# Kernel tuning notes

Hardware: AMD Instinct MI355X
Metric: run time of the kernel (lower is better)

The kernel has to match this reference:

```python
import jax, jax.numpy as jnp
import numpy as np

L = 5        # num_layer
D = 128      # emb_dim
N = 100000   # nodes
E = 500000   # edges
G = 128      # graphs in batch
NUM_TYPES = 100
NUM_ATTRS = 1000
MAX_DEPTH = 21


def _bn(x, g, b):
    # training-mode BatchNorm1d statistics (per-feature over rows)
    mu = x.mean(axis=0)
    var = x.var(axis=0)
    return (x - mu) * jax.lax.rsqrt(var + 1e-5) * g + b


def setup_inputs() -> dict:
    key = jax.random.key(0)
    ks = jax.random.split(key, 24)
    inp = {}
    x0 = jax.random.randint(ks[0], (N,), 0, NUM_TYPES)
    x1 = jax.random.randint(ks[1], (N,), 0, NUM_ATTRS)
    inp['x'] = jnp.stack([x0, x1], axis=1)
    inp['node_depth'] = jax.random.randint(ks[2], (N,), 0, MAX_DEPTH)
    inp['edge_index'] = jax.random.randint(ks[3], (2, E), 0, N)
    inp['batch'] = jnp.sort(jax.random.randint(ks[4], (N,), 0, G))
    inp['edge_attr'] = jax.random.normal(ks[5], (E, 2), dtype=jnp.float32)
    s = 0.02
    inp['type_emb'] = jax.random.normal(ks[6], (NUM_TYPES, D), dtype=jnp.float32) * s
    inp['attr_emb'] = jax.random.normal(ks[7], (NUM_ATTRS, D), dtype=jnp.float32) * s
    inp['depth_emb'] = jax.random.normal(ks[8], (MAX_DEPTH, D), dtype=jnp.float32) * s
    inp['vn_emb'] = jnp.zeros((1, D), dtype=jnp.float32)  # init constant 0
    inp['eps'] = jnp.zeros((L,), dtype=jnp.float32)       # GIN eps
    inp['edge_W'] = jax.random.normal(ks[9], (L, 2, D), dtype=jnp.float32) * s
    inp['edge_b'] = jnp.zeros((L, D), dtype=jnp.float32)
    inp['gin_W1'] = jax.random.normal(ks[10], (L, D, 2 * D), dtype=jnp.float32) * s
    inp['gin_b1'] = jnp.zeros((L, 2 * D), dtype=jnp.float32)
    inp['gin_bng'] = jnp.ones((L, 2 * D), dtype=jnp.float32)
    inp['gin_bnb'] = jnp.zeros((L, 2 * D), dtype=jnp.float32)
    inp['gin_W2'] = jax.random.normal(ks[11], (L, 2 * D, D), dtype=jnp.float32) * s
    inp['gin_b2'] = jnp.zeros((L, D), dtype=jnp.float32)
    inp['bng'] = jnp.ones((L, D), dtype=jnp.float32)
    inp['bnb'] = jnp.zeros((L, D), dtype=jnp.float32)
    inp['vn_W1'] = jax.random.normal(ks[12], (L - 1, D, 2 * D), dtype=jnp.float32) * s
    inp['vn_b1'] = jnp.zeros((L - 1, 2 * D), dtype=jnp.float32)
    inp['vn_bn1g'] = jnp.ones((L - 1, 2 * D), dtype=jnp.float32)
    inp['vn_bn1b'] = jnp.zeros((L - 1, 2 * D), dtype=jnp.float32)
    inp['vn_W2'] = jax.random.normal(ks[13], (L - 1, 2 * D, D), dtype=jnp.float32) * s
    inp['vn_b2'] = jnp.zeros((L - 1, D), dtype=jnp.float32)
    inp['vn_bn2g'] = jnp.ones((L - 1, D), dtype=jnp.float32)
    inp['vn_bn2b'] = jnp.zeros((L - 1, D), dtype=jnp.float32)
    return inp


def reference(x, node_depth, edge_index, batch, edge_attr,
              type_emb, attr_emb, depth_emb, vn_emb, eps,
              edge_W, edge_b, gin_W1, gin_b1, gin_bng, gin_bnb, gin_W2, gin_b2,
              bng, bnb, vn_W1, vn_b1, vn_bn1g, vn_bn1b, vn_W2, vn_b2, vn_bn2g, vn_bn2b):
    # node encoder: type + attribute + depth embeddings  -> [N, D]
    h = type_emb[x[:, 0]] + attr_emb[x[:, 1]] + depth_emb[node_depth]
    vn = jnp.broadcast_to(vn_emb[0], (G, D))  # virtual node per graph
    src, dst = edge_index[0], edge_index[1]
    for l in range(L):
        # broadcast virtual node to its graph's nodes
        h = h + vn[batch]
        # GIN conv: aggr_j relu(h_j + edge_emb), then (1+eps)*h + aggr -> MLP
        eemb = edge_attr @ edge_W[l] + edge_b[l]            # [E, D]
        msg = jax.nn.relu(h[src] + eemb)                    # [E, D]
        aggr = jax.ops.segment_sum(msg, dst, num_segments=N)
        z = (1.0 + eps[l]) * h + aggr
        z = jax.nn.relu(_bn(z @ gin_W1[l] + gin_b1[l], gin_bng[l], gin_bnb[l]))
        z = z @ gin_W2[l] + gin_b2[l]
        hn = _bn(z, bng[l], bnb[l])                         # outer BatchNorm
        if l < L - 1:
            hn = jax.nn.relu(hn)                            # dropout=identity (eval)
            # virtual node update: global_add_pool of pre-conv h + MLP
            vt = jax.ops.segment_sum(h, batch, num_segments=G) + vn
            vt = jax.nn.relu(_bn(vt @ vn_W1[l] + vn_b1[l], vn_bn1g[l], vn_bn1b[l]))
            vn = jax.nn.relu(_bn(vt @ vn_W2[l] + vn_b2[l], vn_bn2g[l], vn_bn2b[l]))
        h = hn
    return h  # JK == 'last'
```

## Files before the change

kernel.cpp:

```cpp
#include <hip/hip_runtime.h>

#define D 128
#define GG 128
#define SLOTS 64

typedef __attribute__((ext_vector_type(8))) short bf16x8;
typedef __attribute__((ext_vector_type(4))) float f32x4;

__device__ __forceinline__ short f2bf(float f) {
  unsigned u = __float_as_uint(f);
  unsigned r = u + 0x7fffu + ((u >> 16) & 1u);
  return (short)(r >> 16);
}
__device__ __forceinline__ float bf2f(unsigned short h) {
  return __uint_as_float(((unsigned)h) << 16);
}

__device__ __forceinline__ void bn_coef(float s, float q, float invn, float g, float b,
                                        float& sc, float& sh) {
  float mu = s * invn;
  float var = q * invn - mu * mu;
  sc = g * rsqrtf(var + 1e-5f);
  sh = b - mu * sc;
}

__global__ void k_deg(int E, const int* __restrict__ dst, int* __restrict__ deg) {
  int e = blockIdx.x * 256 + threadIdx.x;
  if (e < E) atomicAdd(&deg[dst[e]], 1);
}

__global__ void k_scan1(int N, const int* __restrict__ deg,
                        int* __restrict__ incl, int* __restrict__ blksum) {
  __shared__ int s[256];
  int t = threadIdx.x, n = blockIdx.x * 256 + t;
  int v = (n < N) ? deg[n] : 0;
  s[t] = v; __syncthreads();
  for (int off = 1; off < 256; off <<= 1) {
    int x = (t >= off) ? s[t - off] : 0;
    __syncthreads();
    s[t] += x;
    __syncthreads();
  }
  if (n < N) incl[n] = s[t];
  if (t == 255) blksum[blockIdx.x] = s[255];
}

__global__ void k_scan2(int B, int* __restrict__ blksum) {
  __shared__ int s[512];
  int t = threadIdx.x;
  s[t] = (t < B) ? blksum[t] : 0;
  __syncthreads();
  for (int off = 1; off < 512; off <<= 1) {
    int x = (t >= off) ? s[t - off] : 0;
    __syncthreads();
    s[t] += x;
    __syncthreads();
  }
  if (t < B) blksum[t] = s[t];
}

__global__ void k_scan3(int N, const int* __restrict__ incl, const int* __restrict__ blksum,
                        const int* __restrict__ deg, int* __restrict__ row_ptr) {
  int n = blockIdx.x * 256 + threadIdx.x;
  if (n >= N) return;
  int b = n >> 8;
  int off = (b > 0) ? blksum[b - 1] : 0;
  row_ptr[n] = off + incl[n] - deg[n];
  if (n == N - 1) row_ptr[N] = off + incl[n];
}

__global__ void k_fill(int E, const int* __restrict__ src, const int* __restrict__ dst,
                       const float* __restrict__ ea, const int* __restrict__ row_ptr,
                       int* __restrict__ cursor, int* __restrict__ src_sorted,
                       float2* __restrict__ ea_sorted) {
  int e = blockIdx.x * 256 + threadIdx.x;
  if (e >= E) return;
  int d = dst[e];
  int pos = row_ptr[d] + atomicAdd(&cursor[d], 1);
  src_sorted[pos] = src[e];
  ea_sorted[pos] = make_float2(ea[2 * e], ea[2 * e + 1]);
}

__global__ void k_pack(const float* __restrict__ gW1, const float* __restrict__ gW2,
                       short* __restrict__ w1t, short* __restrict__ w2t) {
  int id = blockIdx.x * 256 + threadIdx.x;
  if (id < 5 * 256 * 128) {
    int l = id / 32768, r = id % 32768, n = r / 128, k = r % 128;
    w1t[id] = f2bf(gW1[l * 32768 + k * 256 + n]);
  }
  if (id < 5 * 128 * 256) {
    int l = id / 32768, r = id % 32768, n = r / 256, k = r % 256;
    w2t[id] = f2bf(gW2[l * 32768 + k * 128 + n]);
  }
}

__global__ void k_coef(int NC, float invn,
                       const float* __restrict__ part_s, const float* __restrict__ part_q,
                       const float* __restrict__ g, const float* __restrict__ b,
                       float* __restrict__ sc, float* __restrict__ sh,
                       float* __restrict__ outs, float* __restrict__ outq) {
  int t = threadIdx.x;
  if (t >= NC) return;
  float s = 0.f, q = 0.f;
  #pragma unroll 4
  for (int i = 0; i < SLOTS; ++i) {
    s += part_s[i * NC + t];
    q += part_q[i * NC + t];
  }
  if (outs) { outs[t] = s; outq[t] = q; }
  if (g) {
    float a, c;
    bn_coef(s, q, invn, g[t], b[t], a, c);
    sc[t] = a; sh[t] = c;
  }
}

__global__ void k_nodeprep(int N, int mode,
    const int* __restrict__ x, const int* __restrict__ depth,
    const float* __restrict__ te, const float* __restrict__ ae, const float* __restrict__ de,
    const short* __restrict__ z2, const float* __restrict__ s2, const float* __restrict__ q2,
    const float* __restrict__ g2, const float* __restrict__ b2,
    int vn_mode, const float* __restrict__ vne,
    const float* __restrict__ t2v, const float* __restrict__ vs2, const float* __restrict__ vq2,
    const float* __restrict__ vg2, const float* __restrict__ vb2,
    const int* __restrict__ batch,
    short* __restrict__ h2, float* __restrict__ vt_pool, int do_pool)
{
  int t = threadIdx.x;
  int d = t & (D - 1);
  int lane = t >> 7;
  int n0 = blockIdx.x * 16;
  float invn = 1.0f / (float)N;
  float sc = 0.f, sh = 0.f, vsc = 0.f, vsh = 0.f;
  if (mode == 1)    bn_coef(s2[d], q2[d], invn, g2[d], b2[d], sc, sh);
  if (vn_mode == 1) bn_coef(vs2[d], vq2[d], 1.0f / (float)GG, vg2[d], vb2[d], vsc, vsh);
  int cur = -1; float acc = 0.f;
  for (int k = 0; k < 8; ++k) {
    int n = n0 + lane * 8 + k;
    if (n >= N) break;
    float hv;
    if (mode == 0) {
      hv = te[x[2 * n] * D + d] + ae[x[2 * n + 1] * D + d] + de[depth[n] * D + d];
    } else {
      float z = bf2f((unsigned short)z2[(size_t)n * D + d]);
      hv = fmaxf(z * sc + sh, 0.f);
    }
    int g = batch[n];
    float vnv;
    if (vn_mode == 0) vnv = vne[d];
    else { float tv = t2v[g * D + d]; vnv = fmaxf(tv * vsc + vsh, 0.f); }
    float h = hv + vnv;
    h2[(size_t)n * D + d] = f2bf(h);
    if (do_pool) {
      if (g != cur) {
        if (cur >= 0) atomicAdd(&vt_pool[cur * D + d], acc);
        cur = g; acc = 0.f;
      }
      acc += h;
    }
  }
  if (do_pool && cur >= 0) atomicAdd(&vt_pool[cur * D + d], acc);
}

__global__ void __launch_bounds__(256) k_gather(int N,
    const int* __restrict__ row_ptr, const int* __restrict__ src_sorted,
    const float2* __restrict__ ea_sorted,
    const float* __restrict__ ew, const float* __restrict__ eb,
    const float* __restrict__ epsp,
    const short* __restrict__ h2, short* __restrict__ am)
{
  int t = threadIdx.x;
  int w = t >> 6, l = t & 63;
  int n = blockIdx.x * 4 + w;
  if (n >= N) return;
  int d0 = l * 2;
  float ew00 = ew[d0], ew01 = ew[d0 + 1];
  float ew10 = ew[D + d0], ew11 = ew[D + d0 + 1];
  float eb0 = eb[d0], eb1 = eb[d0 + 1];
  float ep1 = 1.0f + epsp[0];
  unsigned hv = *(const unsigned*)(h2 + (size_t)n * D + d0);
  float acc0 = ep1 * bf2f((unsigned short)(hv & 0xffff));
  float acc1 = ep1 * bf2f((unsigned short)(hv >> 16));
  int beg = row_ptr[n], end = row_ptr[n + 1];
  for (int i = beg; i < end; ++i) {
    int s = src_sorted[i];
    float2 a = ea_sorted[i];
    unsigned sv = *(const unsigned*)(h2 + (size_t)s * D + d0);
    acc0 += fmaxf(bf2f((unsigned short)(sv & 0xffff)) + a.x * ew00 + a.y * ew10 + eb0, 0.f);
    acc1 += fmaxf(bf2f((unsigned short)(sv >> 16))    + a.x * ew01 + a.y * ew11 + eb1, 0.f);
  }
  unsigned o = ((unsigned)(unsigned short)f2bf(acc0)) |
               (((unsigned)(unsigned short)f2bf(acc1)) << 16);
  *(unsigned*)(am + (size_t)n * D + d0) = o;
}

template<int STAGES, int BN_A>
__global__ void __launch_bounds__(256) k_gemm(int N, int NC,
    const short* __restrict__ A, int strideA,
    const short* __restrict__ Bt, int strideB,
    const float* __restrict__ bias,
    const float* __restrict__ scA, const float* __restrict__ shA,
    short* __restrict__ C, int strideC,
    float* __restrict__ part_s, float* __restrict__ part_q)
{
  __shared__ __align__(16) char As[16384];
  __shared__ __align__(16) char Bs[32768];
  __shared__ float cs[128], cq[128];
  int t = threadIdx.x;
  int m0 = blockIdx.x * 64;
  int n0 = blockIdx.y * 128;
  int w = t >> 6, l = t & 63;
  int wr = w & 1, wc = w >> 1;
  int lm = l & 15, kb = l >> 4;

  if (t < 128) { cs[t] = 0.f; cq[t] = 0.f; }

  f32x4 acc[2][4];
  #pragma unroll
  for (int j = 0; j < 4; ++j) {
    float bj = bias[n0 + wc * 64 + j * 16 + lm];
    acc[0][j] = (f32x4){bj, bj, bj, bj};
    acc[1][j] = (f32x4){bj, bj, bj, bj};
  }

  #pragma unroll
  for (int s = 0; s < STAGES; ++s) {
    if (s > 0) __syncthreads();
    #pragma unroll
    for (int r = 0; r < 4; ++r) {
      int p = (r * 256 + t) * 16;
      int row = p >> 8, c = p & 255;
      int gr = m0 + row; if (gr > N - 1) gr = N - 1;
      bf16x8 v = *(const bf16x8*)((const char*)A + (size_t)gr * strideA + s * 256 + c);
      if (BN_A) {
        int kg = s * 128 + (c >> 1);
        float4 s0 = *(const float4*)(scA + kg);
        float4 s1 = *(const float4*)(scA + kg + 4);
        float4 h0 = *(const float4*)(shA + kg);
        float4 h1 = *(const float4*)(shA + kg + 4);
        v[0] = f2bf(fmaxf(bf2f((unsigned short)v[0]) * s0.x + h0.x, 0.f));
        v[1] = f2bf(fmaxf(bf2f((unsigned short)v[1]) * s0.y + h0.y, 0.f));
        v[2] = f2bf(fmaxf(bf2f((unsigned short)v[2]) * s0.z + h0.z, 0.f));
        v[3] = f2bf(fmaxf(bf2f((unsigned short)v[3]) * s0.w + h0.w, 0.f));
        v[4] = f2bf(fmaxf(bf2f((unsigned short)v[4]) * s1.x + h1.x, 0.f));
        v[5] = f2bf(fmaxf(bf2f((unsigned short)v[5]) * s1.y + h1.y, 0.f));
        v[6] = f2bf(fmaxf(bf2f((unsigned short)v[6]) * s1.z + h1.z, 0.f));
        v[7] = f2bf(fmaxf(bf2f((unsigned short)v[7]) * s1.w + h1.w, 0.f));
      }
      *(bf16x8*)(As + row * 256 + (c ^ ((row & 7) << 4))) = v;
    }
    #pragma unroll
    for (int r = 0; r < 8; ++r) {
      int p = (r * 256 + t) * 16;
      int col = p >> 8, c = p & 255;
      bf16x8 v = *(const bf16x8*)((const char*)Bt + (size_t)(n0 + col) * strideB + s * 256 + c);
      *(bf16x8*)(Bs + col * 256 + (c ^ ((col & 7) << 4))) = v;
    }
    __syncthreads();
    #pragma unroll
    for (int ks = 0; ks < 4; ++ks) {
      int kB = ks * 64 + kb * 16;
      bf16x8 fa[2], fb[4];
      #pragma unroll
      for (int i = 0; i < 2; ++i) {
        int rl = wr * 32 + i * 16 + lm;
        fa[i] = *(const bf16x8*)(As + rl * 256 + (kB ^ ((rl & 7) << 4)));
      }
      #pragma unroll
      for (int j = 0; j < 4; ++j) {
        int cl = wc * 64 + j * 16 + lm;
        fb[j] = *(const bf16x8*)(Bs + cl * 256 + (kB ^ ((cl & 7) << 4)));
      }
      #pragma unroll
      for (int i = 0; i < 2; ++i)
        #pragma unroll
        for (int j = 0; j < 4; ++j)
          acc[i][j] = __builtin_amdgcn_mfma_f32_16x16x32_bf16(fa[i], fb[j], acc[i][j], 0, 0, 0);
    }
  }

  #pragma unroll
  for (int j = 0; j < 4; ++j) {
    int col = n0 + wc * 64 + j * 16 + lm;
    float sv = 0.f, qv = 0.f;
    #pragma unroll
    for (int i = 0; i < 2; ++i) {
      #pragma unroll
      for (int r = 0; r < 4; ++r) {
        int row = m0 + wr * 32 + i * 16 + kb * 4 + r;
        float vv = acc[i][j][r];
        if (row < N) { C[(size_t)row * strideC + col] = f2bf(vv); sv += vv; qv += vv * vv; }
      }
    }
    sv += __shfl_xor(sv, 16); sv += __shfl_xor(sv, 32);
    qv += __shfl_xor(qv, 16); qv += __shfl_xor(qv, 32);
    if (l < 16) { atomicAdd(&cs[col - n0], sv); atomicAdd(&cq[col - n0], qv); }
  }
  __syncthreads();
  if (t < 128) {
    int slot = (blockIdx.x + blockIdx.y) & (SLOTS - 1);
    atomicAdd(&part_s[(size_t)slot * NC + n0 + t], cs[t]);
    atomicAdd(&part_q[(size_t)slot * NC + n0 + t], cq[t]);
  }
}

__global__ void k_vn1(const float* __restrict__ vt_pool,
    int vn_mode, const float* __restrict__ vne, const float* __restrict__ t2v,
    const float* __restrict__ vs2, const float* __restrict__ vq2,
    const float* __restrict__ vg2, const float* __restrict__ vb2,
    const float* __restrict__ W1, const float* __restrict__ b1,
    float* __restrict__ t1v, float* __restrict__ s1, float* __restrict__ q1)
{
  __shared__ float vrow[128];
  int g = blockIdx.x, t = threadIdx.x;
  if (t < 128) {
    float vnv;
    if (vn_mode == 0) vnv = vne[t];
    else {
      float sc, sh;
      bn_coef(vs2[t], vq2[t], 1.f / (float)GG, vg2[t], vb2[t], sc, sh);
      vnv = fmaxf(t2v[g * D + t] * sc + sh, 0.f);
    }
    vrow[t] = vt_pool[g * D + t] + vnv;
  }
  __syncthreads();
  float acc = b1[t];
  for (int k = 0; k < 128; ++k) acc += vrow[k] * W1[k * 256 + t];
  t1v[g * 256 + t] = acc;
  atomicAdd(&s1[t], acc);
  atomicAdd(&q1[t], acc * acc);
}

__global__ void k_vn2(const float* __restrict__ t1v,
    const float* __restrict__ s1, const float* __restrict__ q1,
    const float* __restrict__ g1, const float* __restrict__ b1bn,
    const float* __restrict__ W2, const float* __restrict__ b2,
    float* __restrict__ t2v, float* __restrict__ s2, float* __restrict__ q2)
{
  __shared__ float p[256];
  int g = blockIdx.x, t = threadIdx.x;
  for (int u = t; u < 256; u += 128) {
    float sc, sh;
    bn_coef(s1[u], q1[u], 1.f / (float)GG, g1[u], b1bn[u], sc, sh);
    p[u] = fmaxf(t1v[g * 256 + u] * sc + sh, 0.f);
  }
  __syncthreads();
  float acc = b2[t];
  for (int k = 0; k < 256; ++k) acc += p[k] * W2[k * D + t];
  t2v[g * D + t] = acc;
  atomicAdd(&s2[t], acc);
  atomicAdd(&q2[t], acc * acc);
}

__global__ void k_out(int N, const short* __restrict__ z2,
    const float* __restrict__ s2, const float* __restrict__ q2,
    const float* __restrict__ g2, const float* __restrict__ b2, float* __restrict__ out)
{
  long long idx = (long long)blockIdx.x * 256 + threadIdx.x;
  long long base = idx * 2;
  if (base >= (long long)N * D) return;
  int d = (int)(base & (D - 1));
  float invn = 1.f / (float)N;
  unsigned v = *(const unsigned*)(z2 + base);
  float sc0, sh0, sc1, sh1;
  bn_coef(s2[d], q2[d], invn, g2[d], b2[d], sc0, sh0);
  bn_coef(s2[d + 1], q2[d + 1], invn, g2[d + 1], b2[d + 1], sc1, sh1);
  out[base]     = bf2f((unsigned short)(v & 0xffff)) * sc0 + sh0;
  out[base + 1] = bf2f((unsigned short)(v >> 16))    * sc1 + sh1;
}

extern "C" void kernel_launch(void* const* d_in, const int* in_sizes, int n_in,
                              void* d_out, int out_size, void* d_ws, size_t ws_size,
                              hipStream_t stream) {
  const int*   x     = (const int*)d_in[0];
  const int*   depth = (const int*)d_in[1];
  const int*   eidx  = (const int*)d_in[2];
  const int*   batch = (const int*)d_in[3];
  const float* ea    = (const float*)d_in[4];
  const float* te    = (const float*)d_in[5];
  const float* aemb  = (const float*)d_in[6];
  const float* de    = (const float*)d_in[7];
  const float* vne   = (const float*)d_in[8];
  const float* epsp  = (const float*)d_in[9];
  const float* eW    = (const float*)d_in[10];
  const float* eb    = (const float*)d_in[11];
  const float* gW1   = (const float*)d_in[12];
  const float* gb1   = (const float*)d_in[13];
  const float* gbng  = (const float*)d_in[14];
  const float* gbnb  = (const float*)d_in[15];
  const float* gW2   = (const float*)d_in[16];
  const float* gb2   = (const float*)d_in[17];
  const float* bng   = (const float*)d_in[18];
  const float* bnb   = (const float*)d_in[19];
  const float* vW1   = (const float*)d_in[20];
  const float* vb1   = (const float*)d_in[21];
  const float* vbn1g = (const float*)d_in[22];
  const float* vbn1b = (const float*)d_in[23];
  const float* vW2   = (const float*)d_in[24];
  const float* vb2   = (const float*)d_in[25];
  const float* vbn2g = (const float*)d_in[26];
  const float* vbn2b = (const float*)d_in[27];

  int N = in_sizes[0] / 2;
  int E = in_sizes[2] / 2;
  const int* src = eidx;
  const int* dst = eidx + E;

  char* wsp = (char*)d_ws;
  auto alloc = [&](size_t bytes) -> char* {
    char* p = wsp; wsp += (bytes + 15) & ~(size_t)15; return p;
  };
  short* h2         = (short*)alloc((size_t)N * 128 * 2);
  short* am         = (short*)alloc((size_t)N * 128 * 2);
  short* t1         = (short*)alloc((size_t)N * 256 * 2);
  short* z2         = (short*)alloc((size_t)N * 128 * 2);
  short* w1t        = (short*)alloc((size_t)5 * 256 * 128 * 2);
  short* w2t        = (short*)alloc((size_t)5 * 128 * 256 * 2);
  int*   row_ptr    = (int*)alloc((size_t)(N + 1) * 4);
  int*   incl       = (int*)alloc((size_t)N * 4);
  int*   blksum     = (int*)alloc(512 * 4);
  int*   src_sorted = (int*)alloc((size_t)E * 4);
  float2* ea_sorted = (float2*)alloc((size_t)E * 8);
  float* sc1        = (float*)alloc(256 * 4);
  float* sh1        = (float*)alloc(256 * 4);
  char* zero_base = wsp;
  int*  deg    = (int*)alloc((size_t)N * 4);
  int*  cursor = (int*)alloc((size_t)N * 4);
  float* sp = (float*)wsp;
  float *p1s[5], *p1q[5], *p2s[5], *p2q[5], *s2s[5], *q2s[5];
  for (int l = 0; l < 5; ++l) {
    p1s[l]=sp; sp+=SLOTS*256; p1q[l]=sp; sp+=SLOTS*256;
    p2s[l]=sp; sp+=SLOTS*128; p2q[l]=sp; sp+=SLOTS*128;
    s2s[l]=sp; sp+=128; q2s[l]=sp; sp+=128;
  }
  float *vt[4], *t1v[4], *t2v[4], *vs1[4], *vq1[4], *vs2[4], *vq2[4];
  for (int l = 0; l < 4; ++l) {
    vt[l]=sp;  sp+=GG*D;
    t1v[l]=sp; sp+=GG*256;
    t2v[l]=sp; sp+=GG*D;
    vs1[l]=sp; sp+=256; vq1[l]=sp; sp+=256;
    vs2[l]=sp; sp+=128; vq2[l]=sp; sp+=128;
  }
  size_t zero_bytes = (size_t)((char*)sp - zero_base);
  hipMemsetAsync(zero_base, 0, zero_bytes, stream);

  int eblk = (E + 255) / 256;
  int nblk = (N + 255) / 256;
  int B = nblk;
  k_deg<<<eblk, 256, 0, stream>>>(E, dst, deg);
  k_scan1<<<nblk, 256, 0, stream>>>(N, deg, incl, blksum);
  k_scan2<<<1, 512, 0, stream>>>(B, blksum);
  k_scan3<<<nblk, 256, 0, stream>>>(N, incl, blksum, deg, row_ptr);
  k_fill<<<eblk, 256, 0, stream>>>(E, src, dst, ea, row_ptr, cursor, src_sorted, ea_sorted);

  k_pack<<<(5 * 256 * 128 + 255) / 256, 256, 0, stream>>>(gW1, gW2, w1t, w2t);

  int nblk_a = (N + 15) / 16;
  int nblk_gth = (N + 3) / 4;
  int nblk_m = (N + 63) / 64;
  float invn = 1.f / (float)N;

  for (int l = 0; l < 5; ++l) {
    int mode    = (l == 0) ? 0 : 1;
    int vn_mode = (l == 0) ? 0 : 1;
    int do_pool = (l < 4) ? 1 : 0;
    const float* ps2  = (l > 0) ? s2s[l-1] : s2s[0];
    const float* pq2  = (l > 0) ? q2s[l-1] : q2s[0];
    const float* pg2  = (l > 0) ? bng + (l-1)*D : bng;
    const float* pb2  = (l > 0) ? bnb + (l-1)*D : bnb;
    const float* pt2v = (l > 0) ? t2v[l-1] : t2v[0];
    const float* pvs2 = (l > 0) ? vs2[l-1] : vs2[0];
    const float* pvq2 = (l > 0) ? vq2[l-1] : vq2[0];
    const float* pvg2 = (l > 0) ? vbn2g + (l-1)*D : vbn2g;
    const float* pvb2 = (l > 0) ? vbn2b + (l-1)*D : vbn2b;

    k_nodeprep<<<nblk_a, 256, 0, stream>>>(N, mode, x, depth, te, aemb, de,
        z2, ps2, pq2, pg2, pb2,
        vn_mode, vne, pt2v, pvs2, pvq2, pvg2, pvb2,
        batch, h2, do_pool ? vt[l] : vt[0], do_pool);

    k_gather<<<nblk_gth, 256, 0, stream>>>(N, row_ptr, src_sorted, ea_sorted,
        eW + l*2*D, eb + l*D, epsp + l, h2, am);

    k_gemm<1, 0><<<dim3(nblk_m, 2), 256, 0, stream>>>(N, 256,
        am, 256, w1t + (size_t)l*256*128, 256,
        gb1 + l*256, nullptr, nullptr, t1, 256, p1s[l], p1q[l]);

    k_coef<<<1, 256, 0, stream>>>(256, invn, p1s[l], p1q[l],
        gbng + l*256, gbnb + l*256, sc1, sh1, nullptr, nullptr);

    k_gemm<2, 1><<<dim3(nblk_m, 1), 256, 0, stream>>>(N, 128,
        t1, 512, w2t + (size_t)l*128*256, 512,
        gb2 + l*128, sc1, sh1, z2, 128, p2s[l], p2q[l]);

    k_coef<<<1, 256, 0, stream>>>(128, invn, p2s[l], p2q[l],
        nullptr, nullptr, nullptr, nullptr, s2s[l], q2s[l]);

    if (l < 4) {
      k_vn1<<<GG, 256, 0, stream>>>(vt[l], vn_mode, vne, pt2v, pvs2, pvq2, pvg2, pvb2,
          vW1 + (size_t)l*128*256, vb1 + l*256, t1v[l], vs1[l], vq1[l]);
      k_vn2<<<GG, 128, 0, stream>>>(t1v[l], vs1[l], vq1[l],
          vbn1g + l*256, vbn1b + l*256,
          vW2 + (size_t)l*256*128, vb2 + l*128, t2v[l], vs2[l], vq2[l]);
    }
  }

  k_out<<<(int)(((long long)N * D / 2 + 255) / 256), 256, 0, stream>>>(N, z2, s2s[4], q2s[4],
      bng + 4*D, bnb + 4*D, (float*)d_out);
}
```

Measured before the change: 998.3 us.

## Pad CSR to multiples of four, pack edge records, enlarge GEMM tiles, fuse BN coef

Pads each node's in-degree to a multiple of four, using sentinel edges that point at an extra h2 row holding -1e30, so the ReLU of a padded message is zero. Source index and edge attributes are packed into one int4 record per edge, which lets the gather loop unroll by four with fewer index loads. The GEMM tile grows from 64 to 128 rows with launch bounds of 2, and the first BatchNorm coefficient reduction moves into the second GEMM's prologue, removing one k_coef launch per layer. The cost is more gathered bytes per edge (16 vs 12), extra padded iterations, and more registers and LDS per GEMM block. Every second-GEMM block also repeats the 64-slot reduction.

```diff
diff --git a/kernel.cpp b/kernel.cpp
--- a/kernel.cpp
+++ b/kernel.cpp
@@ -33,7 +33,7 @@
                         int* __restrict__ incl, int* __restrict__ blksum) {
   __shared__ int s[256];
   int t = threadIdx.x, n = blockIdx.x * 256 + t;
-  int v = (n < N) ? deg[n] : 0;
+  int v = (n < N) ? ((deg[n] + 3) & ~3) : 0;
   s[t] = v; __syncthreads();
   for (int off = 1; off < 256; off <<= 1) {
     int x = (t >= off) ? s[t - off] : 0;
@@ -65,20 +65,32 @@
   if (n >= N) return;
   int b = n >> 8;
   int off = (b > 0) ? blksum[b - 1] : 0;
-  row_ptr[n] = off + incl[n] - deg[n];
+  int pdeg = (deg[n] + 3) & ~3;
+  row_ptr[n] = off + incl[n] - pdeg;
   if (n == N - 1) row_ptr[N] = off + incl[n];
 }
 
 __global__ void k_fill(int E, const int* __restrict__ src, const int* __restrict__ dst,
                        const float* __restrict__ ea, const int* __restrict__ row_ptr,
-                       int* __restrict__ cursor, int* __restrict__ src_sorted,
-                       float2* __restrict__ ea_sorted) {
+                       int* __restrict__ cursor, int4* __restrict__ er) {
   int e = blockIdx.x * 256 + threadIdx.x;
   if (e >= E) return;
   int d = dst[e];
   int pos = row_ptr[d] + atomicAdd(&cursor[d], 1);
-  src_sorted[pos] = src[e];
-  ea_sorted[pos] = make_float2(ea[2 * e], ea[2 * e + 1]);
+  er[pos] = make_int4(src[e] << 8, __float_as_int(ea[2 * e]), __float_as_int(ea[2 * e + 1]), 0);
+}
+
+__global__ void k_padfill(int N, const int* __restrict__ deg, const int* __restrict__ row_ptr,
+                          int4* __restrict__ er) {
+  int n = blockIdx.x * 256 + threadIdx.x;
+  if (n >= N) return;
+  int s = row_ptr[n] + deg[n], e = row_ptr[n + 1];
+  int4 pad = make_int4(N << 8, 0, 0, 0);
+  for (int p = s; p < e; ++p) er[p] = pad;
+}
+
+__global__ void k_sentinel(int N, short* __restrict__ h2) {
+  h2[(size_t)N * D + threadIdx.x] = f2bf(-1e30f);
 }
 
 __global__ void k_pack(const float* __restrict__ gW1, const float* __restrict__ gW2,
@@ -94,10 +106,8 @@
   }
 }
 
-__global__ void k_coef(int NC, float invn,
+__global__ void k_coef(int NC,
                        const float* __restrict__ part_s, const float* __restrict__ part_q,
-                       const float* __restrict__ g, const float* __restrict__ b,
-                       float* __restrict__ sc, float* __restrict__ sh,
                        float* __restrict__ outs, float* __restrict__ outq) {
   int t = threadIdx.x;
   if (t >= NC) return;
@@ -107,12 +117,7 @@
     s += part_s[i * NC + t];
     q += part_q[i * NC + t];
   }
-  if (outs) { outs[t] = s; outq[t] = q; }
-  if (g) {
-    float a, c;
-    bn_coef(s, q, invn, g[t], b[t], a, c);
-    sc[t] = a; sh[t] = c;
-  }
+  outs[t] = s; outq[t] = q;
 }
 
 __global__ void k_nodeprep(int N, int mode,
@@ -163,8 +168,7 @@
 }
 
 __global__ void __launch_bounds__(256) k_gather(int N,
-    const int* __restrict__ row_ptr, const int* __restrict__ src_sorted,
-    const float2* __restrict__ ea_sorted,
+    const int* __restrict__ row_ptr, const int4* __restrict__ er,
     const float* __restrict__ ew, const float* __restrict__ eb,
     const float* __restrict__ epsp,
     const short* __restrict__ h2, short* __restrict__ am)
@@ -173,21 +177,35 @@
   int w = t >> 6, l = t & 63;
   int n = blockIdx.x * 4 + w;
   if (n >= N) return;
+  const char* h2b = (const char*)h2;
+  int lb = l << 2;
   int d0 = l * 2;
   float ew00 = ew[d0], ew01 = ew[d0 + 1];
   float ew10 = ew[D + d0], ew11 = ew[D + d0 + 1];
   float eb0 = eb[d0], eb1 = eb[d0 + 1];
   float ep1 = 1.0f + epsp[0];
-  unsigned hv = *(const unsigned*)(h2 + (size_t)n * D + d0);
+  unsigned hv = *(const unsigned*)(h2b + ((size_t)n << 8) + lb);
   float acc0 = ep1 * bf2f((unsigned short)(hv & 0xffff));
   float acc1 = ep1 * bf2f((unsigned short)(hv >> 16));
   int beg = row_ptr[n], end = row_ptr[n + 1];
-  for (int i = beg; i < end; ++i) {
-    int s = src_sorted[i];
-    float2 a = ea_sorted[i];
-    unsigned sv = *(const unsigned*)(h2 + (size_t)s * D + d0);
-    acc0 += fmaxf(bf2f((unsigned short)(sv & 0xffff)) + a.x * ew00 + a.y * ew10 + eb0, 0.f);
-    acc1 += fmaxf(bf2f((unsigned short)(sv >> 16))    + a.x * ew01 + a.y * ew11 + eb1, 0.f);
+  for (int i = beg; i < end; i += 4) {
+    int4 e0 = er[i], e1 = er[i + 1], e2 = er[i + 2], e3 = er[i + 3];
+    unsigned v0 = *(const unsigned*)(h2b + e0.x + lb);
+    unsigned v1 = *(const unsigned*)(h2b + e1.x + lb);
+    unsigned v2 = *(const unsigned*)(h2b + e2.x + lb);
+    unsigned v3 = *(const unsigned*)(h2b + e3.x + lb);
+    float a0x = __int_as_float(e0.y), a0y = __int_as_float(e0.z);
+    float a1x = __int_as_float(e1.y), a1y = __int_as_float(e1.z);
+    float a2x = __int_as_float(e2.y), a2y = __int_as_float(e2.z);
+    float a3x = __int_as_float(e3.y), a3y = __int_as_float(e3.z);
+    acc0 += fmaxf(bf2f((unsigned short)(v0 & 0xffff)) + a0x * ew00 + a0y * ew10 + eb0, 0.f);
+    acc1 += fmaxf(bf2f((unsigned short)(v0 >> 16))    + a0x * ew01 + a0y * ew11 + eb1, 0.f);
+    acc0 += fmaxf(bf2f((unsigned short)(v1 & 0xffff)) + a1x * ew00 + a1y * ew10 + eb0, 0.f);
+    acc1 += fmaxf(bf2f((unsigned short)(v1 >> 16))    + a1x * ew01 + a1y * ew11 + eb1, 0.f);
+    acc0 += fmaxf(bf2f((unsigned short)(v2 & 0xffff)) + a2x * ew00 + a2y * ew10 + eb0, 0.f);
+    acc1 += fmaxf(bf2f((unsigned short)(v2 >> 16))    + a2x * ew01 + a2y * ew11 + eb1, 0.f);
+    acc0 += fmaxf(bf2f((unsigned short)(v3 & 0xffff)) + a3x * ew00 + a3y * ew10 + eb0, 0.f);
+    acc1 += fmaxf(bf2f((unsigned short)(v3 >> 16))    + a3x * ew01 + a3y * ew11 + eb1, 0.f);
   }
   unsigned o = ((unsigned)(unsigned short)f2bf(acc0)) |
                (((unsigned)(unsigned short)f2bf(acc1)) << 16);
@@ -195,49 +213,63 @@
 }
 
 template<int STAGES, int BN_A>
-__global__ void __launch_bounds__(256) k_gemm(int N, int NC,
+__global__ void __launch_bounds__(256, 2) k_gemm(int N, int NC, float invn,
     const short* __restrict__ A, int strideA,
     const short* __restrict__ Bt, int strideB,
     const float* __restrict__ bias,
-    const float* __restrict__ scA, const float* __restrict__ shA,
+    const float* __restrict__ pAs, const float* __restrict__ pAq,
+    const float* __restrict__ g1, const float* __restrict__ b1,
     short* __restrict__ C, int strideC,
     float* __restrict__ part_s, float* __restrict__ part_q)
 {
-  __shared__ __align__(16) char As[16384];
+  __shared__ __align__(16) char As[32768];
   __shared__ __align__(16) char Bs[32768];
+  __shared__ float scs[256], shs[256];
   __shared__ float cs[128], cq[128];
   int t = threadIdx.x;
-  int m0 = blockIdx.x * 64;
+  int m0 = blockIdx.x * 128;
   int n0 = blockIdx.y * 128;
   int w = t >> 6, l = t & 63;
-  int wr = w & 1, wc = w >> 1;
+  int wr = w >> 1, wc = w & 1;
   int lm = l & 15, kb = l >> 4;
 
   if (t < 128) { cs[t] = 0.f; cq[t] = 0.f; }
-
-  f32x4 acc[2][4];
+  if (BN_A) {
+    float s = 0.f, q = 0.f;
+    #pragma unroll 4
+    for (int i = 0; i < SLOTS; ++i) {
+      s += pAs[i * 256 + t];
+      q += pAq[i * 256 + t];
+    }
+    float a, c;
+    bn_coef(s, q, invn, g1[t], b1[t], a, c);
+    scs[t] = a; shs[t] = c;
+  }
+  __syncthreads();
+
+  f32x4 acc[4][4];
   #pragma unroll
   for (int j = 0; j < 4; ++j) {
     float bj = bias[n0 + wc * 64 + j * 16 + lm];
-    acc[0][j] = (f32x4){bj, bj, bj, bj};
-    acc[1][j] = (f32x4){bj, bj, bj, bj};
+    #pragma unroll
+    for (int i = 0; i < 4; ++i) acc[i][j] = (f32x4){bj, bj, bj, bj};
   }
 
   #pragma unroll
   for (int s = 0; s < STAGES; ++s) {
     if (s > 0) __syncthreads();
     #pragma unroll
-    for (int r = 0; r < 4; ++r) {
+    for (int r = 0; r < 8; ++r) {
       int p = (r * 256 + t) * 16;
       int row = p >> 8, c = p & 255;
       int gr = m0 + row; if (gr > N - 1) gr = N - 1;
       bf16x8 v = *(const bf16x8*)((const char*)A + (size_t)gr * strideA + s * 256 + c);
       if (BN_A) {
         int kg = s * 128 + (c >> 1);
-        float4 s0 = *(const float4*)(scA + kg);
-        float4 s1 = *(const float4*)(scA + kg + 4);
-        float4 h0 = *(const float4*)(shA + kg);
-        float4 h1 = *(const float4*)(shA + kg + 4);
+        float4 s0 = *(const float4*)(scs + kg);
+        float4 s1 = *(const float4*)(scs + kg + 4);
+        float4 h0 = *(const float4*)(shs + kg);
+        float4 h1 = *(const float4*)(shs + kg + 4);
         v[0] = f2bf(fmaxf(bf2f((unsigned short)v[0]) * s0.x + h0.x, 0.f));
         v[1] = f2bf(fmaxf(bf2f((unsigned short)v[1]) * s0.y + h0.y, 0.f));
         v[2] = f2bf(fmaxf(bf2f((unsigned short)v[2]) * s0.z + h0.z, 0.f));
@@ -260,10 +292,10 @@
     #pragma unroll
     for (int ks = 0; ks < 4; ++ks) {
       int kB = ks * 64 + kb * 16;
-      bf16x8 fa[2], fb[4];
+      bf16x8 fa[4], fb[4];
       #pragma unroll
-      for (int i = 0; i < 2; ++i) {
-        int rl = wr * 32 + i * 16 + lm;
+      for (int i = 0; i < 4; ++i) {
+        int rl = wr * 64 + i * 16 + lm;
         fa[i] = *(const bf16x8*)(As + rl * 256 + (kB ^ ((rl & 7) << 4)));
       }
       #pragma unroll
@@ -272,7 +304,7 @@
         fb[j] = *(const bf16x8*)(Bs + cl * 256 + (kB ^ ((cl & 7) << 4)));
       }
       #pragma unroll
-      for (int i = 0; i < 2; ++i)
+      for (int i = 0; i < 4; ++i)
         #pragma unroll
         for (int j = 0; j < 4; ++j)
           acc[i][j] = __builtin_amdgcn_mfma_f32_16x16x32_bf16(fa[i], fb[j], acc[i][j], 0, 0, 0);
@@ -284,10 +316,10 @@
     int col = n0 + wc * 64 + j * 16 + lm;
     float sv = 0.f, qv = 0.f;
     #pragma unroll
-    for (int i = 0; i < 2; ++i) {
+    for (int i = 0; i < 4; ++i) {
       #pragma unroll
       for (int r = 0; r < 4; ++r) {
-        int row = m0 + wr * 32 + i * 16 + kb * 4 + r;
+        int row = m0 + wr * 64 + i * 16 + kb * 4 + r;
         float vv = acc[i][j][r];
         if (row < N) { C[(size_t)row * strideC + col] = f2bf(vv); sv += vv; qv += vv * vv; }
       }
@@ -410,7 +442,7 @@
   auto alloc = [&](size_t bytes) -> char* {
     char* p = wsp; wsp += (bytes + 15) & ~(size_t)15; return p;
   };
-  short* h2         = (short*)alloc((size_t)N * 128 * 2);
+  short* h2         = (short*)alloc((size_t)(N + 1) * 128 * 2);
   short* am         = (short*)alloc((size_t)N * 128 * 2);
   short* t1         = (short*)alloc((size_t)N * 256 * 2);
   short* z2         = (short*)alloc((size_t)N * 128 * 2);
@@ -419,10 +451,7 @@
   int*   row_ptr    = (int*)alloc((size_t)(N + 1) * 4);
   int*   incl       = (int*)alloc((size_t)N * 4);
   int*   blksum     = (int*)alloc(512 * 4);
-  int*   src_sorted = (int*)alloc((size_t)E * 4);
-  float2* ea_sorted = (float2*)alloc((size_t)E * 8);
-  float* sc1        = (float*)alloc(256 * 4);
-  float* sh1        = (float*)alloc(256 * 4);
+  int4*  er         = (int4*)alloc(((size_t)E + 3 * (size_t)N + 16) * 16);
   char* zero_base = wsp;
   int*  deg    = (int*)alloc((size_t)N * 4);
   int*  cursor = (int*)alloc((size_t)N * 4);
@@ -451,13 +480,15 @@
   k_scan1<<<nblk, 256, 0, stream>>>(N, deg, incl, blksum);
   k_scan2<<<1, 512, 0, stream>>>(B, blksum);
   k_scan3<<<nblk, 256, 0, stream>>>(N, incl, blksum, deg, row_ptr);
-  k_fill<<<eblk, 256, 0, stream>>>(E, src, dst, ea, row_ptr, cursor, src_sorted, ea_sorted);
+  k_fill<<<eblk, 256, 0, stream>>>(E, src, dst, ea, row_ptr, cursor, er);
+  k_padfill<<<nblk, 256, 0, stream>>>(N, deg, row_ptr, er);
+  k_sentinel<<<1, 128, 0, stream>>>(N, h2);
 
   k_pack<<<(5 * 256 * 128 + 255) / 256, 256, 0, stream>>>(gW1, gW2, w1t, w2t);
 
   int nblk_a = (N + 15) / 16;
   int nblk_gth = (N + 3) / 4;
-  int nblk_m = (N + 63) / 64;
+  int nblk_m = (N + 127) / 128;
   float invn = 1.f / (float)N;
 
   for (int l = 0; l < 5; ++l) {
@@ -479,22 +510,20 @@
         vn_mode, vne, pt2v, pvs2, pvq2, pvg2, pvb2,
         batch, h2, do_pool ? vt[l] : vt[0], do_pool);
 
-    k_gather<<<nblk_gth, 256, 0, stream>>>(N, row_ptr, src_sorted, ea_sorted,
+    k_gather<<<nblk_gth, 256, 0, stream>>>(N, row_ptr, er,
         eW + l*2*D, eb + l*D, epsp + l, h2, am);
 
-    k_gemm<1, 0><<<dim3(nblk_m, 2), 256, 0, stream>>>(N, 256,
+    k_gemm<1, 0><<<dim3(nblk_m, 2), 256, 0, stream>>>(N, 256, invn,
         am, 256, w1t + (size_t)l*256*128, 256,
-        gb1 + l*256, nullptr, nullptr, t1, 256, p1s[l], p1q[l]);
-
-    k_coef<<<1, 256, 0, stream>>>(256, invn, p1s[l], p1q[l],
-        gbng + l*256, gbnb + l*256, sc1, sh1, nullptr, nullptr);
-
-    k_gemm<2, 1><<<dim3(nblk_m, 1), 256, 0, stream>>>(N, 128,
+        gb1 + l*256, nullptr, nullptr, nullptr, nullptr,
+        t1, 256, p1s[l], p1q[l]);
+
+    k_gemm<2, 1><<<dim3(nblk_m, 1), 256, 0, stream>>>(N, 128, invn,
         t1, 512, w2t + (size_t)l*128*256, 512,
-        gb2 + l*128, sc1, sh1, z2, 128, p2s[l], p2q[l]);
-
-    k_coef<<<1, 256, 0, stream>>>(128, invn, p2s[l], p2q[l],
-        nullptr, nullptr, nullptr, nullptr, s2s[l], q2s[l]);
+        gb2 + l*128, p1s[l], p1q[l], gbng + l*256, gbnb + l*256,
+        z2, 128, p2s[l], p2q[l]);
+
+    k_coef<<<1, 128, 0, stream>>>(128, p2s[l], p2q[l], s2s[l], q2s[l]);
 
     if (l < 4) {
       k_vn1<<<GG, 256, 0, stream>>>(vt[l], vn_mode, vne, pt2v, pvs2, pvq2, pvg2, pvb2,
```

New measurement: 910.2 us. -8.8%, faster.
